# Kernel tuning notes

Hardware: AMD Instinct MI355X
Metric: run time of the kernel (lower is better)

The kernel has to match this reference:

```python
import jax, jax.numpy as jnp
import numpy as np
import math

L = 6        # num_layers
H = 16       # nhead
D = 1024     # feature_dim (= d_model, dim_factor=1)
DFF = 1024
IN = 1024    # input_dim
B, T = 16, 512
HD = D // H
EPS = 1e-5


def _get_slopes(n):
    def pow2(n):
        start = 2.0 ** (-2.0 ** (-(math.log2(n) - 3)))
        return [start * (start ** i) for i in range(n)]
    if math.log2(n).is_integer():
        return pow2(n)
    cp2 = 2 ** math.floor(math.log2(n))
    return pow2(cp2) + _get_slopes(2 * cp2)[0::2][: n - cp2]


def _alibi_bias(num_heads, seq_len):
    # init_alibi_biased_mask_future reduces to -slope_h * |i - j|
    slopes = jnp.asarray(_get_slopes(num_heads), dtype=jnp.float32)  # [H]
    idx = jnp.arange(seq_len)
    rel = -jnp.abs(idx[:, None] - idx[None, :]).astype(jnp.float32)  # [T,T]
    return slopes[:, None, None] * rel  # [H,T,T]


def _ln(x, w, b):
    m = jnp.mean(x, axis=-1, keepdims=True)
    v = jnp.mean(jnp.square(x - m), axis=-1, keepdims=True)
    return (x - m) * jax.lax.rsqrt(v + EPS) * w + b


def setup_inputs() -> dict:
    key = jax.random.key(0)
    ks = jax.random.split(key, 16)
    s = 0.02
    return {
        "x": jax.random.normal(ks[0], (B, T, IN), dtype=jnp.float32),
        "bn_w": jax.random.normal(ks[1], (D, IN), dtype=jnp.float32) * s,
        "bn_b": jnp.zeros((D,), jnp.float32),
        "qkv_w": jax.random.normal(ks[2], (L, 3 * D, D), dtype=jnp.float32) * s,
        "qkv_b": jnp.zeros((L, 3 * D), jnp.float32),
        "out_w": jax.random.normal(ks[3], (L, D, D), dtype=jnp.float32) * s,
        "out_b": jnp.zeros((L, D), jnp.float32),
        "ln1_w": jnp.ones((L, D), jnp.float32),
        "ln1_b": jnp.zeros((L, D), jnp.float32),
        "ln2_w": jnp.ones((L, D), jnp.float32),
        "ln2_b": jnp.zeros((L, D), jnp.float32),
        "ff1_w": jax.random.normal(ks[4], (L, DFF, D), dtype=jnp.float32) * s,
        "ff1_b": jnp.zeros((L, DFF), jnp.float32),
        "ff2_w": jax.random.normal(ks[5], (L, D, DFF), dtype=jnp.float32) * s,
        "ff2_b": jnp.zeros((L, D), jnp.float32),
    }


def reference(x, bn_w, bn_b, qkv_w, qkv_b, out_w, out_b,
              ln1_w, ln1_b, ln2_w, ln2_b, ff1_w, ff1_b, ff2_w, ff2_b):
    b, t, _ = x.shape
    bias = _alibi_bias(H, t)  # [H,T,T], same for all batch elements
    h = x @ bn_w.T + bn_b  # bottleneck -> [B,T,D]
    scale = 1.0 / math.sqrt(HD)
    for l in range(L):
        qkv = h @ qkv_w[l].T + qkv_b[l]  # [B,T,3D]
        q, k, v = jnp.split(qkv, 3, axis=-1)
        q = q.reshape(b, t, H, HD)
        k = k.reshape(b, t, H, HD)
        v = v.reshape(b, t, H, HD)
        scores = jnp.einsum('bihd,bjhd->bhij', q, k) * scale + bias[None]
        attn = jax.nn.softmax(scores, axis=-1)
        o = jnp.einsum('bhij,bjhd->bihd', attn, v).reshape(b, t, D)
        o = o @ out_w[l].T + out_b[l]
        h = _ln(h + o, ln1_w[l], ln1_b[l])  # post-norm (PyTorch default)
        f = jax.nn.gelu(h @ ff1_w[l].T + ff1_b[l], approximate=False)
        f = f @ ff2_w[l].T + ff2_b[l]
        h = _ln(h + f, ln2_w[l], ln2_b[l])
    return h
```

## Files before the change

kernel.cpp:

```cpp
#include <hip/hip_runtime.h>
#include <stdint.h>

#define DEV static __device__ __forceinline__

typedef __attribute__((ext_vector_type(8))) uint16_t u16x8;
typedef __attribute__((ext_vector_type(4))) uint16_t u16x4;
typedef __attribute__((ext_vector_type(4))) uint32_t u32x4;
typedef __attribute__((ext_vector_type(4))) float    f32x4;
typedef __attribute__((ext_vector_type(8))) __bf16   bf16x8;

typedef __attribute__((address_space(3))) void lds_void;
typedef __attribute__((address_space(1))) void gbl_void;

DEV float bf2f(uint16_t u){
  union { uint32_t i; float f; } v; v.i = ((uint32_t)u) << 16; return v.f;
}
DEV uint16_t f2bf(float f){ return __builtin_bit_cast(uint16_t, (__bf16)f); }
DEV f32x4 mfma16(u16x8 a, u16x8 b, f32x4 c){
  return __builtin_amdgcn_mfma_f32_16x16x32_bf16(
      __builtin_bit_cast(bf16x8, a), __builtin_bit_cast(bf16x8, b), c, 0, 0, 0);
}
DEV uint32_t cvt_pk_bf16(float lo, float hi){
  uint32_t r;
  asm("v_cvt_pk_bf16_f32 %0, %1, %2" : "=v"(r) : "v"(lo), "v"(hi));
  return r;
}

__global__ __launch_bounds__(256)
void te_cvt(const float* __restrict__ in, uint16_t* __restrict__ out)
{
  const size_t i = ((size_t)blockIdx.x * 256 + threadIdx.x) * 8;
  f32x4 a = *(const f32x4*)(in + i);
  f32x4 b = *(const f32x4*)(in + i + 4);
  u16x8 o;
#pragma unroll
  for (int e = 0; e < 4; e++) {
    o[e]     = f2bf(a[e]);
    o[e + 4] = f2bf(b[e]);
  }
  *(u16x8*)(out + i) = o;
}

__global__ __launch_bounds__(256)
void te_gemm_bb(const uint16_t* __restrict__ A, int lda,
                const uint16_t* __restrict__ W, const float* __restrict__ bias,
                uint16_t* __restrict__ outB, int M, int N, int K)
{
  __shared__ uint16_t la[128 * 64];
  __shared__ uint16_t lb[128 * 64];
  const int tid = threadIdx.x;
  const int w = tid >> 6, l = tid & 63;
  const int lr = l & 15, lg = l >> 4;
  const int tm = blockIdx.y * 128, tn = blockIdx.x * 128;
  const int srow = l >> 3;
  const int scol = ((l & 7) ^ srow) * 8;
  const int wr = (w >> 1) * 64, wc = (w & 1) * 64;

  f32x4 acc[4][4] = {};

  for (int k0 = 0; k0 < K; k0 += 64) {
#pragma unroll
    for (int c = 0; c < 4; c++) {
      const int rb = (c * 4 + w) * 8;
      const uint16_t* ga = A + (size_t)(tm + rb + srow) * lda + (k0 + scol);
      __builtin_amdgcn_global_load_lds((gbl_void*)(uintptr_t)ga,
                                       (lds_void*)(la + rb * 64), 16, 0, 0);
      const uint16_t* gw = W + (size_t)(tn + rb + srow) * K + (k0 + scol);
      __builtin_amdgcn_global_load_lds((gbl_void*)(uintptr_t)gw,
                                       (lds_void*)(lb + rb * 64), 16, 0, 0);
    }
    __syncthreads();
#pragma unroll
    for (int kk = 0; kk < 2; kk++) {
      u16x8 af[4], bfr[4];
#pragma unroll
      for (int i = 0; i < 4; i++) {
        const int row = wr + i * 16 + lr;
        af[i] = *(const u16x8*)&la[row * 64 + (((kk * 4 + lg) ^ (lr & 7)) << 3)];
      }
#pragma unroll
      for (int j = 0; j < 4; j++) {
        const int row = wc + j * 16 + lr;
        bfr[j] = *(const u16x8*)&lb[row * 64 + (((kk * 4 + lg) ^ (lr & 7)) << 3)];
      }
      __builtin_amdgcn_s_setprio(1);
#pragma unroll
      for (int i = 0; i < 4; i++)
#pragma unroll
        for (int j = 0; j < 4; j++)
          acc[i][j] = mfma16(af[i], bfr[j], acc[i][j]);
      __builtin_amdgcn_s_setprio(0);
    }
    __syncthreads();
  }

  float bv[4];
#pragma unroll
  for (int j = 0; j < 4; j++) bv[j] = bias[tn + wc + j * 16 + lr];
#pragma unroll
  for (int i = 0; i < 4; i++)
#pragma unroll
    for (int j = 0; j < 4; j++)
#pragma unroll
      for (int r = 0; r < 4; r++) {
        const int row = tm + wr + i * 16 + lg * 4 + r;
        const int col = tn + wc + j * 16 + lr;
        float v = acc[i][j][r] + bv[j];
        outB[(size_t)row * N + col] = f2bf(v);
      }
}

template<int MODE>
__global__ __launch_bounds__(512)
void te_gemm256(const uint16_t* __restrict__ A, int lda,
                const uint16_t* __restrict__ Wm, const float* __restrict__ bias,
                uint16_t* __restrict__ outB, int N, int K)
{
  constexpr int SZA = 256 * 64;
  constexpr int SZB = 128 * 64;
  __shared__ uint16_t lds[3 * (SZA + SZB)];

  const int tid = threadIdx.x;
  const int w = tid >> 6, l = tid & 63;
  const int lr = l & 15, lg = l >> 4;
  const int wr = w >> 1, wc = w & 1;
  const int srow = l >> 3, chunk = l & 7;

  const int nb = gridDim.x;
  const int bid = blockIdx.x;
  const int lid = (bid & 7) * (nb >> 3) + (bid >> 3);
  const int nx = N >> 7;
  const int tm = (lid / nx) << 8;
  const int tn = (lid % nx) << 7;

  const int rw = w * 8 + srow;
  const int sc = (chunk ^ srow) << 3;

  auto stage = [&](int kt, int p) {
    const int k0 = kt << 6;
    uint16_t* bufA = lds + p * (SZA + SZB);
    uint16_t* bufB = bufA + SZA;
#pragma unroll
    for (int c = 0; c < 4; c++) {
      const uint16_t* ga = A + (size_t)(tm + c * 64 + rw) * lda + (k0 + sc);
      __builtin_amdgcn_global_load_lds((gbl_void*)(uintptr_t)ga,
          (lds_void*)(bufA + (c * 64 + w * 8) * 64), 16, 0, 0);
    }
#pragma unroll
    for (int c = 0; c < 2; c++) {
      const uint16_t* gw = Wm + (size_t)(tn + c * 64 + rw) * K + (k0 + sc);
      __builtin_amdgcn_global_load_lds((gbl_void*)(uintptr_t)gw,
          (lds_void*)(bufB + (c * 64 + w * 8) * 64), 16, 0, 0);
    }
  };

  f32x4 acc[4][4] = {};
  const int nt = K >> 6;

  stage(0, 0);
  stage(1, 1);
  for (int t = 0; t < nt; ++t) {
    const int cur = t % 3;
    uint16_t* bufA = lds + cur * (SZA + SZB);
    uint16_t* bufB = bufA + SZA;

    asm volatile("" ::: "memory");
    if (t + 2 < nt) {
      stage(t + 2, (t + 2) % 3);
      asm volatile("s_waitcnt vmcnt(12)" ::: "memory");
    } else if (t + 1 < nt) {
      asm volatile("s_waitcnt vmcnt(6)" ::: "memory");
    } else {
      asm volatile("s_waitcnt vmcnt(0)" ::: "memory");
    }
    __builtin_amdgcn_s_barrier();

#pragma unroll
    for (int kk = 0; kk < 2; kk++) {
      u16x8 af[4], bfr[2];
#pragma unroll
      for (int i = 0; i < 4; i++) {
        const int row = wr * 64 + i * 16 + lr;
        af[i] = *(const u16x8*)&bufA[row * 64 + (((kk * 4 + lg) ^ (lr & 7)) << 3)];
      }
#pragma unroll
      for (int j = 0; j < 2; j++) {
        const int row = wc * 64 + j * 16 + lr;
        bfr[j] = *(const u16x8*)&bufB[row * 64 + (((kk * 4 + lg) ^ (lr & 7)) << 3)];
      }
      u16x8 bfr2[2];
#pragma unroll
      for (int j = 0; j < 2; j++) {
        const int row = wc * 64 + (j + 2) * 16 + lr;
        bfr2[j] = *(const u16x8*)&bufB[row * 64 + (((kk * 4 + lg) ^ (lr & 7)) << 3)];
      }
      __builtin_amdgcn_s_setprio(1);
#pragma unroll
      for (int i = 0; i < 4; i++) {
        acc[i][0] = mfma16(af[i], bfr[0],  acc[i][0]);
        acc[i][1] = mfma16(af[i], bfr[1],  acc[i][1]);
        acc[i][2] = mfma16(af[i], bfr2[0], acc[i][2]);
        acc[i][3] = mfma16(af[i], bfr2[1], acc[i][3]);
      }
      __builtin_amdgcn_s_setprio(0);
    }
    __builtin_amdgcn_s_barrier();
  }

  float bv[4];
#pragma unroll
  for (int j = 0; j < 4; j++) bv[j] = bias[tn + wc * 64 + j * 16 + lr];
#pragma unroll
  for (int i = 0; i < 4; i++)
#pragma unroll
    for (int j = 0; j < 4; j++)
#pragma unroll
      for (int r = 0; r < 4; r++) {
        const int row = tm + wr * 64 + i * 16 + lg * 4 + r;
        const int col = tn + wc * 64 + j * 16 + lr;
        float v = acc[i][j][r] + bv[j];
        if (MODE == 2) {
          const float u = 0.7978845608028654f * v * (1.0f + 0.044715f * v * v);
          const float t = 1.0f - 2.0f / (__expf(2.0f * u) + 1.0f);
          v = 0.5f * v * (1.0f + t);
        }
        outB[(size_t)row * N + col] = f2bf(v);
      }
}

#define SOFTMAX_PACK(S, MR, SDQ, ACC, IQ, P2)                                  \
  {                                                                            \
    const float f0 = (float)((IQ) - jt - lg * 4);                              \
    float mt = -1e30f;                                                         \
    _Pragma("unroll")                                                          \
    for (int n = 0; n < 4; n++) {                                              \
      const float fj = f0 - (float)(n * 16);                                   \
      _Pragma("unroll")                                                        \
      for (int r = 0; r < 4; r++) {                                            \
        const float v = fmaf(S[n][r], scl2e, -slope2e * fabsf(fj - (float)r)); \
        S[n][r] = v;                                                           \
        mt = fmaxf(mt, v);                                                     \
      }                                                                        \
    }                                                                          \
    mt = fmaxf(mt, __shfl_xor(mt, 16));                                        \
    mt = fmaxf(mt, __shfl_xor(mt, 32));                                        \
    if (!__all(mt <= MR)) {                                                    \
      const float mN = fmaxf(MR, mt);                                          \
      const float fq = exp2f(MR - mN);                                         \
      MR = mN;                                                                 \
      SDQ *= fq;                                                               \
      float fA[4];                                                             \
      _Pragma("unroll")                                                        \
      for (int r = 0; r < 4; r++) fA[r] = __shfl(fq, lg * 4 + r);              \
      _Pragma("unroll")                                                        \
      for (int n = 0; n < 4; n++)                                              \
        _Pragma("unroll")                                                      \
        for (int r = 0; r < 4; r++) ACC[n][r] *= fA[r];                        \
    }                                                                          \
    float rs = 0.0f;                                                           \
    _Pragma("unroll")                                                          \
    for (int n = 0; n < 4; n++)                                                \
      _Pragma("unroll")                                                        \
      for (int r = 0; r < 4; r++) {                                            \
        const float p = exp2f(S[n][r] - MR);                                   \
        S[n][r] = p;                                                           \
        rs += p;                                                               \
      }                                                                        \
    rs += __shfl_xor(rs, 16);                                                  \
    rs += __shfl_xor(rs, 32);                                                  \
    SDQ += rs;                                                                 \
    _Pragma("unroll")                                                          \
    for (int n = 0; n < 4; n++) {                                              \
      P2[n][0] = cvt_pk_bf16(S[n][0], S[n][1]);                                \
      P2[n][1] = cvt_pk_bf16(S[n][2], S[n][3]);                                \
    }                                                                          \
  }

__global__ __launch_bounds__(256)
void te_attn(uint16_t* __restrict__ qkv)
{
  __shared__ uint16_t kl[64 * 64];
  __shared__ uint16_t vt[64 * 64];
  const int tid = threadIdx.x;
  const int w = tid >> 6, l = tid & 63;
  const int lr = l & 15, lg = l >> 4;
  const int bh = blockIdx.x, qt = blockIdx.y;
  const int h = bh & 15, b = bh >> 4;

  const int iQ0 = qt * 128 + w * 16 + lr;
  u16x8 qf[2][2];
#pragma unroll
  for (int g = 0; g < 2; g++) {
    const size_t qoff = ((size_t)(b * 512 + iQ0 + g * 64)) * 3072 + h * 64 + lg * 8;
    qf[g][0] = *(const u16x8*)&qkv[qoff];
    qf[g][1] = *(const u16x8*)&qkv[qoff + 32];
  }
  const float LOG2E = 1.4426950408889634f;
  const float scl2e = 0.125f * LOG2E;
  const float slope2e = exp2f(-0.5f * (float)(h + 1)) * LOG2E;

  const int sjb = tid >> 3;
  const int sd0 = (tid & 7) * 8;

  float mR0 = -1e30f, sdq0 = 0.0f, mR1 = -1e30f, sdq1 = 0.0f;
  f32x4 acc0[4] = {}, acc1[4] = {};

  u16x8 kreg[2], vreg[2];
  {
    const int jt0 = (qt * 2) * 64;
#pragma unroll
    for (int cc = 0; cc < 2; cc++) {
      const int j = sjb + cc * 32;
      const size_t rbase = ((size_t)(b * 512 + jt0 + j)) * 3072 + h * 64 + sd0;
      kreg[cc] = *(const u16x8*)&qkv[rbase + 1024];
      vreg[cc] = *(const u16x8*)&qkv[rbase + 2048];
    }
  }

  for (int step = 0; step < 8; step++) {
    const int jt = ((qt * 2 + step) & 7) * 64;
#pragma unroll
    for (int cc = 0; cc < 2; cc++) {
      const int j = sjb + cc * 32;
      *(u16x8*)&kl[j * 64 + (((sd0 >> 3) ^ (j & 7)) << 3)] = kreg[cc];
      const int cV = (((j >> 3) ^ (sd0 >> 3)) << 3) + (j & 7);
#pragma unroll
      for (int e = 0; e < 8; e++) vt[(sd0 + e) * 64 + cV] = vreg[cc][e];
    }
    __syncthreads();
    if (step < 7) {
      const int jtn = ((qt * 2 + step + 1) & 7) * 64;
#pragma unroll
      for (int cc = 0; cc < 2; cc++) {
        const int j = sjb + cc * 32;
        const size_t rbase = ((size_t)(b * 512 + jtn + j)) * 3072 + h * 64 + sd0;
        kreg[cc] = *(const u16x8*)&qkv[rbase + 1024];
        vreg[cc] = *(const u16x8*)&qkv[rbase + 2048];
      }
    }

    f32x4 s0[4] = {}, s1[4] = {};
#pragma unroll
    for (int kk = 0; kk < 2; kk++) {
      u16x8 kf[4];
#pragma unroll
      for (int n = 0; n < 4; n++) {
        const int row = n * 16 + lr;
        kf[n] = *(const u16x8*)&kl[row * 64 + (((kk * 4 + lg) ^ (lr & 7)) << 3)];
      }
      __builtin_amdgcn_s_setprio(1);
#pragma unroll
      for (int n = 0; n < 4; n++) {
        s0[n] = mfma16(kf[n], qf[0][kk], s0[n]);
        s1[n] = mfma16(kf[n], qf[1][kk], s1[n]);
      }
      __builtin_amdgcn_s_setprio(0);
    }

    uint32_t P2a[4][2], P2b[4][2];
    SOFTMAX_PACK(s0, mR0, sdq0, acc0, iQ0,      P2a);
    SOFTMAX_PACK(s1, mR1, sdq1, acc1, iQ0 + 64, P2b);

#pragma unroll
    for (int kk = 0; kk < 2; kk++) {
      uint32_t pw0[4], pw1[4];
#pragma unroll
      for (int t = 0; t < 4; t++) {
        const int srcLane = lr + 16 * ((lg & 1) * 2 + (t >> 1));
        const uint32_t a0 = __shfl(P2a[2 * kk + 0][t & 1], srcLane);
        const uint32_t b0 = __shfl(P2a[2 * kk + 1][t & 1], srcLane);
        pw0[t] = (lg >> 1) ? b0 : a0;
        const uint32_t a1 = __shfl(P2b[2 * kk + 0][t & 1], srcLane);
        const uint32_t b1 = __shfl(P2b[2 * kk + 1][t & 1], srcLane);
        pw1[t] = (lg >> 1) ? b1 : a1;
      }
      u32x4 q0 = { pw0[0], pw0[1], pw0[2], pw0[3] };
      u32x4 q1 = { pw1[0], pw1[1], pw1[2], pw1[3] };
      u16x8 pf0 = __builtin_bit_cast(u16x8, q0);
      u16x8 pf1 = __builtin_bit_cast(u16x8, q1);
      u16x8 vf[4];
#pragma unroll
      for (int n = 0; n < 4; n++) {
        const int row = n * 16 + lr;
        vf[n] = *(const u16x8*)&vt[row * 64 + ((((kk * 4 + lg) ^ (2 * n + (lr >> 3))) & 7) << 3)];
      }
      __builtin_amdgcn_s_setprio(1);
#pragma unroll
      for (int n = 0; n < 4; n++) {
        acc0[n] = mfma16(pf0, vf[n], acc0[n]);
        acc1[n] = mfma16(pf1, vf[n], acc1[n]);
      }
      __builtin_amdgcn_s_setprio(0);
    }
    __syncthreads();
  }

  {
    float sdA[4];
#pragma unroll
    for (int r = 0; r < 4; r++) sdA[r] = 1.0f / __shfl(sdq0, lg * 4 + r);
#pragma unroll
    for (int n = 0; n < 4; n++)
#pragma unroll
      for (int r = 0; r < 4; r++) {
        const int i = qt * 128 + w * 16 + lg * 4 + r;
        const int d = h * 64 + n * 16 + lr;
        qkv[((size_t)(b * 512 + i)) * 3072 + d] = f2bf(acc0[n][r] * sdA[r]);
      }
  }
  {
    float sdA[4];
#pragma unroll
    for (int r = 0; r < 4; r++) sdA[r] = 1.0f / __shfl(sdq1, lg * 4 + r);
#pragma unroll
    for (int n = 0; n < 4; n++)
#pragma unroll
      for (int r = 0; r < 4; r++) {
        const int i = qt * 128 + 64 + w * 16 + lg * 4 + r;
        const int d = h * 64 + n * 16 + lr;
        qkv[((size_t)(b * 512 + i)) * 3072 + d] = f2bf(acc1[n][r] * sdA[r]);
      }
  }
}

template<int FINAL>
__global__ __launch_bounds__(256)
void te_ln(const uint16_t* __restrict__ h, const uint16_t* __restrict__ delta,
           const float* __restrict__ w, const float* __restrict__ b,
           uint16_t* __restrict__ hout, float* __restrict__ fout)
{
  const int row = blockIdx.x, t = threadIdx.x;
  const size_t base = (size_t)row * 1024 + t * 4;
  u16x4 hv = *(const u16x4*)&h[base];
  u16x4 dv = *(const u16x4*)&delta[base];
  float x[4];
#pragma unroll
  for (int i = 0; i < 4; i++) x[i] = bf2f(hv[i]) + bf2f(dv[i]);
  float s = x[0] + x[1] + x[2] + x[3];
  float ss = x[0]*x[0] + x[1]*x[1] + x[2]*x[2] + x[3]*x[3];
#pragma unroll
  for (int msk = 32; msk >= 1; msk >>= 1) {
    s  += __shfl_xor(s, msk);
    ss += __shfl_xor(ss, msk);
  }
  __shared__ float rs[4], rq[4];
  const int wv = t >> 6;
  if ((t & 63) == 0) { rs[wv] = s; rq[wv] = ss; }
  __syncthreads();
  s  = rs[0] + rs[1] + rs[2] + rs[3];
  ss = rq[0] + rq[1] + rq[2] + rq[3];
  const float mean = s * (1.0f / 1024.0f);
  const float var  = ss * (1.0f / 1024.0f) - mean * mean;
  const float rstd = rsqrtf(var + 1e-5f);
  f32x4 wv4 = *(const f32x4*)&w[t * 4];
  f32x4 bv4 = *(const f32x4*)&b[t * 4];
  if (FINAL == 0) {
    u16x4 bo;
#pragma unroll
    for (int i = 0; i < 4; i++)
      bo[i] = f2bf((x[i] - mean) * rstd * wv4[i] + bv4[i]);
    *(u16x4*)&hout[base] = bo;
  } else {
    f32x4 yo;
#pragma unroll
    for (int i = 0; i < 4; i++)
      yo[i] = (x[i] - mean) * rstd * wv4[i] + bv4[i];
    *(f32x4*)&fout[base] = yo;
  }
}

extern "C" void kernel_launch(void* const* d_in, const int* in_sizes, int n_in,
                              void* d_out, int out_size, void* d_ws, size_t ws_size,
                              hipStream_t stream)
{
  (void)in_sizes; (void)n_in; (void)out_size; (void)ws_size;
  const float* x     = (const float*)d_in[0];
  const float* bn_w  = (const float*)d_in[1];
  const float* bn_b  = (const float*)d_in[2];
  const float* qkv_w = (const float*)d_in[3];
  const float* qkv_b = (const float*)d_in[4];
  const float* out_w = (const float*)d_in[5];
  const float* out_b = (const float*)d_in[6];
  const float* ln1_w = (const float*)d_in[7];
  const float* ln1_b = (const float*)d_in[8];
  const float* ln2_w = (const float*)d_in[9];
  const float* ln2_b = (const float*)d_in[10];
  const float* ff1_w = (const float*)d_in[11];
  const float* ff1_b = (const float*)d_in[12];
  const float* ff2_w = (const float*)d_in[13];
  const float* ff2_b = (const float*)d_in[14];

  char* ws = (char*)d_ws;
  uint16_t* h_bf    = (uint16_t*)ws;
  uint16_t* qkvb    = (uint16_t*)(ws + (16u  << 20));
  uint16_t* scrA    = (uint16_t*)(ws + (64u  << 20));
  uint16_t* qkvw_bf = (uint16_t*)(ws + (80u  << 20));
  uint16_t* ff2w_bf = (uint16_t*)(ws + (116u << 20));
  uint16_t* bnw_bf  = (uint16_t*)(ws + (128u << 20));
  uint16_t* outw_bf = (uint16_t*)d_out;
  uint16_t* ff1w_bf = (uint16_t*)((char*)d_out + (12u << 20));
  float*    outf    = (float*)d_out;

  dim3 blk(256);
  dim3 blk512(512);

  te_cvt<<<dim3(18874368 / 2048), blk, 0, stream>>>(qkv_w, qkvw_bf);
  te_cvt<<<dim3(6291456  / 2048), blk, 0, stream>>>(out_w, outw_bf);
  te_cvt<<<dim3(6291456  / 2048), blk, 0, stream>>>(ff1_w, ff1w_bf);
  te_cvt<<<dim3(6291456  / 2048), blk, 0, stream>>>(ff2_w, ff2w_bf);
  te_cvt<<<dim3(1048576  / 2048), blk, 0, stream>>>(bn_w,  bnw_bf);
  te_cvt<<<dim3(8388608  / 2048), blk, 0, stream>>>(x,     scrA);

  te_gemm256<0><<<dim3(256), blk512, 0, stream>>>(scrA, 1024, bnw_bf, bn_b,
                                                  h_bf, 1024, 1024);

  for (int l = 0; l < 6; l++) {
    te_gemm_bb<<<dim3(24, 64), blk, 0, stream>>>(
        h_bf, 1024, qkvw_bf + (size_t)l * 3072 * 1024, qkv_b + l * 3072,
        qkvb, 8192, 3072, 1024);
    te_attn<<<dim3(256, 4), blk, 0, stream>>>(qkvb);
    te_gemm256<0><<<dim3(256), blk512, 0, stream>>>(
        qkvb, 3072, outw_bf + (size_t)l * 1024 * 1024, out_b + l * 1024,
        scrA, 1024, 1024);
    te_ln<0><<<dim3(8192), blk, 0, stream>>>(h_bf, scrA, ln1_w + l * 1024, ln1_b + l * 1024,
                                             h_bf, nullptr);
    te_gemm256<2><<<dim3(256), blk512, 0, stream>>>(
        h_bf, 1024, ff1w_bf + (size_t)l * 1024 * 1024, ff1_b + l * 1024,
        scrA, 1024, 1024);
    te_gemm256<0><<<dim3(256), blk512, 0, stream>>>(
        scrA, 1024, ff2w_bf + (size_t)l * 1024 * 1024, ff2_b + l * 1024,
        qkvb, 1024, 1024);
    if (l == 5) {
      te_ln<1><<<dim3(8192), blk, 0, stream>>>(h_bf, qkvb, ln2_w + l * 1024, ln2_b + l * 1024,
                                               nullptr, outf);
    } else {
      te_ln<0><<<dim3(8192), blk, 0, stream>>>(h_bf, qkvb, ln2_w + l * 1024, ln2_b + l * 1024,
                                               h_bf, nullptr);
    }
  }
}
```

Baseline: 1.423 ms.

## Fuse conversion launches, remap QKV GEMM blocks per XCD, double-buffer attention K/V

```diff
diff --git a/kernel.cpp b/kernel.cpp
--- a/kernel.cpp
+++ b/kernel.cpp
@@ -27,18 +27,33 @@
 }
 
 __global__ __launch_bounds__(256)
-void te_cvt(const float* __restrict__ in, uint16_t* __restrict__ out)
+void te_cvt_all(const float* __restrict__ qkv_w, const float* __restrict__ out_w,
+                const float* __restrict__ ff1_w, const float* __restrict__ ff2_w,
+                const float* __restrict__ bn_w,  const float* __restrict__ x,
+                uint16_t* __restrict__ qkvw_bf, uint16_t* __restrict__ outw_bf,
+                uint16_t* __restrict__ ff1w_bf, uint16_t* __restrict__ ff2w_bf,
+                uint16_t* __restrict__ bnw_bf,  uint16_t* __restrict__ x_bf)
 {
-  const size_t i = ((size_t)blockIdx.x * 256 + threadIdx.x) * 8;
-  f32x4 a = *(const f32x4*)(in + i);
-  f32x4 b = *(const f32x4*)(in + i + 4);
-  u16x8 o;
-#pragma unroll
-  for (int e = 0; e < 4; e++) {
-    o[e]     = f2bf(a[e]);
-    o[e + 4] = f2bf(b[e]);
-  }
-  *(u16x8*)(out + i) = o;
+  const size_t TOTAL = 47185920u;
+  const size_t stride = (size_t)gridDim.x * 2048;
+  for (size_t i = ((size_t)blockIdx.x * 256 + threadIdx.x) * 8; i < TOTAL; i += stride) {
+    const float* src; uint16_t* dst; size_t off;
+    if      (i < 18874368u) { src = qkv_w; dst = qkvw_bf; off = i; }
+    else if (i < 25165824u) { src = out_w; dst = outw_bf; off = i - 18874368u; }
+    else if (i < 31457280u) { src = ff1_w; dst = ff1w_bf; off = i - 25165824u; }
+    else if (i < 37748736u) { src = ff2_w; dst = ff2w_bf; off = i - 31457280u; }
+    else if (i < 38797312u) { src = bn_w;  dst = bnw_bf;  off = i - 37748736u; }
+    else                    { src = x;     dst = x_bf;    off = i - 38797312u; }
+    f32x4 a = *(const f32x4*)(src + off);
+    f32x4 b = *(const f32x4*)(src + off + 4);
+    u16x8 o;
+#pragma unroll
+    for (int e = 0; e < 4; e++) {
+      o[e]     = f2bf(a[e]);
+      o[e + 4] = f2bf(b[e]);
+    }
+    *(u16x8*)(dst + off) = o;
+  }
 }
 
 __global__ __launch_bounds__(256)
@@ -51,7 +66,14 @@
   const int tid = threadIdx.x;
   const int w = tid >> 6, l = tid & 63;
   const int lr = l & 15, lg = l >> 4;
-  const int tm = blockIdx.y * 128, tn = blockIdx.x * 128;
+
+  const int nb = gridDim.x;
+  const int id = blockIdx.x;
+  const int lid = (id & 7) * (nb >> 3) + (id >> 3);
+  const int nx = N >> 7;
+  const int tm = (lid / nx) << 7;
+  const int tn = (lid % nx) << 7;
+
   const int srow = l >> 3;
   const int scol = ((l & 7) ^ srow) * 8;
   const int wr = (w >> 1) * 64, wc = (w & 1) * 64;
@@ -279,8 +301,8 @@
 __global__ __launch_bounds__(256)
 void te_attn(uint16_t* __restrict__ qkv)
 {
-  __shared__ uint16_t kl[64 * 64];
-  __shared__ uint16_t vt[64 * 64];
+  __shared__ uint16_t kl[2][64 * 64];
+  __shared__ uint16_t vt[2][64 * 64];
   const int tid = threadIdx.x;
   const int w = tid >> 6, l = tid & 63;
   const int lr = l & 15, lg = l >> 4;
@@ -306,37 +328,38 @@
   f32x4 acc0[4] = {}, acc1[4] = {};
 
   u16x8 kreg[2], vreg[2];
-  {
-    const int jt0 = (qt * 2) * 64;
+  auto loadKV = [&](int step) {
+    const int jtl = ((qt * 2 + step) & 7) * 64;
 #pragma unroll
     for (int cc = 0; cc < 2; cc++) {
       const int j = sjb + cc * 32;
-      const size_t rbase = ((size_t)(b * 512 + jt0 + j)) * 3072 + h * 64 + sd0;
+      const size_t rbase = ((size_t)(b * 512 + jtl + j)) * 3072 + h * 64 + sd0;
       kreg[cc] = *(const u16x8*)&qkv[rbase + 1024];
       vreg[cc] = *(const u16x8*)&qkv[rbase + 2048];
     }
-  }
+  };
+  auto writeKV = [&](int buf) {
+#pragma unroll
+    for (int cc = 0; cc < 2; cc++) {
+      const int j = sjb + cc * 32;
+      *(u16x8*)&kl[buf][j * 64 + (((sd0 >> 3) ^ (j & 7)) << 3)] = kreg[cc];
+      const int cV = (((j >> 3) ^ (sd0 >> 3)) << 3) + (j & 7);
+#pragma unroll
+      for (int e = 0; e < 8; e++) vt[buf][(sd0 + e) * 64 + cV] = vreg[cc][e];
+    }
+  };
+
+  loadKV(0);
+  writeKV(0);
+  loadKV(1);
 
   for (int step = 0; step < 8; step++) {
     const int jt = ((qt * 2 + step) & 7) * 64;
-#pragma unroll
-    for (int cc = 0; cc < 2; cc++) {
-      const int j = sjb + cc * 32;
-      *(u16x8*)&kl[j * 64 + (((sd0 >> 3) ^ (j & 7)) << 3)] = kreg[cc];
-      const int cV = (((j >> 3) ^ (sd0 >> 3)) << 3) + (j & 7);
-#pragma unroll
-      for (int e = 0; e < 8; e++) vt[(sd0 + e) * 64 + cV] = vreg[cc][e];
-    }
+    const int cur = step & 1;
     __syncthreads();
     if (step < 7) {
-      const int jtn = ((qt * 2 + step + 1) & 7) * 64;
-#pragma unroll
-      for (int cc = 0; cc < 2; cc++) {
-        const int j = sjb + cc * 32;
-        const size_t rbase = ((size_t)(b * 512 + jtn + j)) * 3072 + h * 64 + sd0;
-        kreg[cc] = *(const u16x8*)&qkv[rbase + 1024];
-        vreg[cc] = *(const u16x8*)&qkv[rbase + 2048];
-      }
+      writeKV(cur ^ 1);
+      if (step < 6) loadKV(step + 2);
     }
 
     f32x4 s0[4] = {}, s1[4] = {};
@@ -346,7 +369,7 @@
 #pragma unroll
       for (int n = 0; n < 4; n++) {
         const int row = n * 16 + lr;
-        kf[n] = *(const u16x8*)&kl[row * 64 + (((kk * 4 + lg) ^ (lr & 7)) << 3)];
+        kf[n] = *(const u16x8*)&kl[cur][row * 64 + (((kk * 4 + lg) ^ (lr & 7)) << 3)];
       }
       __builtin_amdgcn_s_setprio(1);
 #pragma unroll
@@ -382,7 +405,7 @@
 #pragma unroll
       for (int n = 0; n < 4; n++) {
         const int row = n * 16 + lr;
-        vf[n] = *(const u16x8*)&vt[row * 64 + ((((kk * 4 + lg) ^ (2 * n + (lr >> 3))) & 7) << 3)];
+        vf[n] = *(const u16x8*)&vt[cur][row * 64 + ((((kk * 4 + lg) ^ (2 * n + (lr >> 3))) & 7) << 3)];
       }
       __builtin_amdgcn_s_setprio(1);
 #pragma unroll
@@ -392,7 +415,6 @@
       }
       __builtin_amdgcn_s_setprio(0);
     }
-    __syncthreads();
   }
 
   {
@@ -504,18 +526,15 @@
   dim3 blk(256);
   dim3 blk512(512);
 
-  te_cvt<<<dim3(18874368 / 2048), blk, 0, stream>>>(qkv_w, qkvw_bf);
-  te_cvt<<<dim3(6291456  / 2048), blk, 0, stream>>>(out_w, outw_bf);
-  te_cvt<<<dim3(6291456  / 2048), blk, 0, stream>>>(ff1_w, ff1w_bf);
-  te_cvt<<<dim3(6291456  / 2048), blk, 0, stream>>>(ff2_w, ff2w_bf);
-  te_cvt<<<dim3(1048576  / 2048), blk, 0, stream>>>(bn_w,  bnw_bf);
-  te_cvt<<<dim3(8388608  / 2048), blk, 0, stream>>>(x,     scrA);
+  te_cvt_all<<<dim3(5760), blk, 0, stream>>>(qkv_w, out_w, ff1_w, ff2_w, bn_w, x,
+                                             qkvw_bf, outw_bf, ff1w_bf, ff2w_bf,
+                                             bnw_bf, scrA);
 
   te_gemm256<0><<<dim3(256), blk512, 0, stream>>>(scrA, 1024, bnw_bf, bn_b,
                                                   h_bf, 1024, 1024);
 
   for (int l = 0; l < 6; l++) {
-    te_gemm_bb<<<dim3(24, 64), blk, 0, stream>>>(
+    te_gemm_bb<<<dim3(1536), blk, 0, stream>>>(
         h_bf, 1024, qkvw_bf + (size_t)l * 3072 * 1024, qkv_b + l * 3072,
         qkvb, 8192, 3072, 1024);
     te_attn<<<dim3(256, 4), blk, 0, stream>>>(qkvb);
```

Result: faster. 1.395 ms (-2.0%).
